# Optimization experiments

Hardware: AMD Instinct MI355X
Metric: run time of the kernel (lower is better)

The kernel has to match this reference:

```python
import jax, jax.numpy as jnp
import numpy as np

# Winograd F(2x2, 3x3) transform matrices (standard Lavin & Gray form).
# The original torch module encodes B^T / A^T but applies them with elementwise
# mul (a bug that crashes); the intended math is Y = A^T [ (G g G^T) .* (B^T d B) ] A
# per 4x4 input tile with stride 2, which equals a valid 3x3 conv. We implement
# that intended Winograd computation faithfully and vectorized.
_BT = jnp.array([[1., 0., -1., 0.],
                 [0., 1., 1., 0.],
                 [0., -1., 1., 0.],
                 [0., 1., 0., -1.]], dtype=jnp.float32)
_G = jnp.array([[1., 0., 0.],
                [0.5, 0.5, 0.5],
                [0.5, -0.5, 0.5],
                [0., 0., 1.]], dtype=jnp.float32)
_AT = jnp.array([[1., 1., 1., 0.],
                 [0., 1., -1., -1.]], dtype=jnp.float32)


def setup_inputs() -> dict:
    key = jax.random.key(0)
    k1, k2 = jax.random.split(key)
    X = jax.random.normal(k1, (16, 32, 258, 258), dtype=jnp.float32)
    K = jax.random.normal(k2, (32, 32, 3, 3), dtype=jnp.float32)
    return {"X": X, "K": K}


def _winograd_conv(X, K):
    B_, C, H, W = X.shape
    Fo = K.shape[0]
    blocks = (H - 3) // 2 + 1  # number of 2x2 output tiles per spatial dim

    # Kernel transform: U = G K G^T  -> (Fo, C, 4, 4)
    U = jnp.einsum('ij,fcjk,lk->fcil', _G, K, _G)

    # Extract overlapping 4x4 tiles with stride 2: (B, C, blocks, blocks, 4, 4)
    i0 = jnp.arange(blocks) * 2
    win = i0[:, None] + jnp.arange(4)[None, :]          # (blocks, 4)
    tiles = X[:, :, win, :]                              # (B, C, blocks, 4, W)
    tiles = tiles[:, :, :, :, win]                       # (B, C, blocks, 4, blocks, 4)
    tiles = tiles.transpose(0, 1, 2, 4, 3, 5)            # (B, C, p, q, 4, 4)

    # Input transform: V = B^T d B
    V = jnp.einsum('ij,bcpqjk,lk->bcpqil', _BT, tiles, _BT)

    # Elementwise multiply in transform domain, summed over input channels
    M = jnp.einsum('fcil,bcpqil->bfpqil', U, V)          # (B, Fo, p, q, 4, 4)

    # Inverse transform: Y = A^T M A -> (B, Fo, p, q, 2, 2)
    Y = jnp.einsum('ij,bfpqjk,lk->bfpqil', _AT, M, _AT)

    # Stitch 2x2 tiles back: (B, Fo, 2*blocks, 2*blocks)
    out = Y.transpose(0, 1, 2, 4, 3, 5).reshape(B_, Fo, 2 * blocks, 2 * blocks)
    return out


def reference(X, K):
    return _winograd_conv(X, K)
```

## Files before the change

kernel.cpp:

```cpp
#include <hip/hip_runtime.h>
#include <stdint.h>

typedef __attribute__((ext_vector_type(8))) short bf16x8;
typedef __attribute__((ext_vector_type(4))) float f32x4;
typedef __attribute__((ext_vector_type(2))) float f32x2;

__device__ inline float bflo(uint32_t w) { union { uint32_t i; float f; } v; v.i = w << 16; return v.f; }
__device__ inline float bfhi(uint32_t w) { union { uint32_t i; float f; } v; v.i = w & 0xffff0000u; return v.f; }
__device__ inline uint32_t f2bf(float f) { union { float f; uint32_t i; } v; v.f = f; return (v.i + 0x8000u) >> 16; }
__device__ inline uint32_t pk(float lo, float hi) { return f2bf(lo) | (f2bf(hi) << 16); }

__device__ inline f32x2 pka(f32x2 a, f32x2 b) {
    f32x2 d; asm("v_pk_add_f32 %0, %1, %2" : "=v"(d) : "v"(a), "v"(b)); return d;
}
__device__ inline f32x2 pks(f32x2 a, f32x2 b) {
    f32x2 d; asm("v_pk_add_f32 %0, %1, %2 neg_lo:[0,1] neg_hi:[0,1]" : "=v"(d) : "v"(a), "v"(b)); return d;
}
__device__ inline uint32_t cvtpk2(float lo, float hi) {
    uint32_t r; asm("v_cvt_pk_bf16_f32 %0, %1, %2" : "=v"(r) : "v"(lo), "v"(hi)); return r;
}
__device__ inline uint32_t cvtpk(f32x2 v) { return cvtpk2(v.x, v.y); }
__device__ inline f32x2 unpk(uint32_t w) {
    union { uint32_t u; float f; } lo, hi; lo.u = w << 16; hi.u = w & 0xffff0000u;
    return (f32x2){lo.f, hi.f};
}

__global__ __launch_bounds__(256) void wg_filter(const float* __restrict__ Kk, uint32_t* __restrict__ Ud)
{
    const int idx = blockIdx.x * 256 + threadIdx.x;
    if (idx >= 512) return;
    const int cp = idx & 15, f = idx >> 4;
    float u[2][16];
    #pragma unroll
    for (int h = 0; h < 2; h++) {
        const float* kp = Kk + (f * 32 + cp * 2 + h) * 9;
        float k00 = kp[0], k01 = kp[1], k02 = kp[2];
        float k10 = kp[3], k11 = kp[4], k12 = kp[5];
        float k20 = kp[6], k21 = kp[7], k22 = kp[8];
        float t[4][3];
        t[0][0] = k00; t[0][1] = k01; t[0][2] = k02;
        t[1][0] = 0.5f * (k00 + k10 + k20); t[1][1] = 0.5f * (k01 + k11 + k21); t[1][2] = 0.5f * (k02 + k12 + k22);
        t[2][0] = 0.5f * (k00 - k10 + k20); t[2][1] = 0.5f * (k01 - k11 + k21); t[2][2] = 0.5f * (k02 - k12 + k22);
        t[3][0] = k20; t[3][1] = k21; t[3][2] = k22;
        #pragma unroll
        for (int i = 0; i < 4; i++) {
            float a0 = t[i][0], a1 = t[i][1], a2 = t[i][2];
            u[h][i * 4 + 0] = a0;
            u[h][i * 4 + 1] = 0.5f * (a0 + a1 + a2);
            u[h][i * 4 + 2] = 0.5f * (a0 - a1 + a2);
            u[h][i * 4 + 3] = a2;
        }
    }
    const int base = ((cp >> 2) * 32 + f) * 4 + (cp & 3);
    #pragma unroll
    for (int p = 0; p < 16; p++) Ud[p * 512 + base] = pk(u[0][p], u[1][p]);
}

template<int CH>
__device__ __forceinline__ void d_phase(const uint16_t* __restrict__ Vbuf,
                                        const bf16x8 (&a)[4], float (&y)[4][4],
                                        int tb, int lq, int l15)
{
    const uint16_t* Vb = Vbuf + ((tb * 4 + lq) * 16 + l15) * 8;
    f32x4 acc[4];
    #pragma unroll
    for (int l = 0; l < 4; l++) {
        bf16x8 v = *(const bf16x8*)(Vb + l * 1024);
        acc[l] = __builtin_amdgcn_mfma_f32_16x16x32_bf16(a[l], v,
                    (f32x4){0.f, 0.f, 0.f, 0.f}, 0, 0, 0);
    }
    #pragma unroll
    for (int r = 0; r < 4; r++) {
        float m0 = acc[0][r], m1 = acc[1][r], m2 = acc[2][r], m3 = acc[3][r];
        float c0 = m0 + m1 + m2, c1 = m1 - m2 - m3;
        if (CH == 0)      { y[r][0] += c0; y[r][1] += c1; }
        else if (CH == 1) { y[r][0] += c0; y[r][1] += c1; y[r][2] += c0; y[r][3] += c1; }
        else if (CH == 2) { y[r][0] += c0; y[r][1] += c1; y[r][2] -= c0; y[r][3] -= c1; }
        else              { y[r][2] -= c0; y[r][3] -= c1; }
    }
}

__global__ __launch_bounds__(256, 3) void wg_main(
    const float* __restrict__ X, const uint16_t* __restrict__ U, float* __restrict__ out)
{
    __shared__ __align__(16) uint32_t Pl[2912];
    __shared__ __align__(16) uint16_t Vl[2][4096];

    const int tid = threadIdx.x;
    const int lin  = blockIdx.x + 16 * (blockIdx.y + 32 * blockIdx.z);
    const int work = (lin & 7) * 1024 + (lin >> 3);
    const int qb = work & 15;
    const int pb = (work >> 4) & 31;
    const int b  = work >> 9;
    const int y0 = pb * 8, x0 = qb * 16;

    const int wave = tid >> 6, lane = tid & 63;
    const int fh = wave & 1, tb = wave >> 1;
    const int l15 = lane & 15, lq = lane >> 4;
    const uint16_t* Ub = U + (lq * 32 + fh * 16 + l15) * 8;

    bf16x8 a_cur[4], a_nxt[4];
    #pragma unroll
    for (int l = 0; l < 4; l++)
        a_cur[l] = *(const bf16x8*)(Ub + l * 1024);

    for (int s = tid; s < 1440; s += 256) {
        const int pr = s / 90;
        const int r  = s - pr * 90;
        const int row = r / 9, seg = r - row * 9;
        const float* g0 = X + ((size_t)((b * 32 + pr * 2) * 258 + y0 + row)) * 258 + x0 + seg * 2;
        float2 a = *(const float2*)g0;
        float2 c = *(const float2*)(g0 + 258 * 258);
        uint2 w;
        w.x = cvtpk2(a.x, c.x);
        w.y = cvtpk2(a.y, c.y);
        *(uint2*)&Pl[pr * 182 + row * 18 + seg * 2] = w;
    }
    #pragma unroll
    for (int l = 0; l < 4; l++)
        a_nxt[l] = *(const bf16x8*)(Ub + (2 * 4 + l) * 1024);
    __syncthreads();

    const int cp2 = tid & 3, t15c = (tid >> 2) & 15;

    float y[4][4];
    #pragma unroll
    for (int r = 0; r < 4; r++)
        #pragma unroll
        for (int j = 0; j < 4; j++) y[r][j] = 0.f;

    uint32_t vh1[2][4], vh3[2][4];
    int vbs[2];
    uint32_t* vp0 = (uint32_t*)Vl[0];
    uint32_t* vp1 = (uint32_t*)Vl[1];

    #pragma unroll
    for (int it = 0; it < 2; it++) {
        const int rem  = it * 4 + wave;
        const int tblk = rem & 1, cpH = rem >> 1;
        const int cp   = cpH * 4 + cp2;
        const int tt   = tblk * 16 + t15c;
        const int tr   = tt >> 3, tc = tt & 7;
        const uint32_t* pp = &Pl[cp * 182 + (tr * 2) * 18 + tc * 2];
        f32x2 d[4][4];
        #pragma unroll
        for (int j = 0; j < 4; j++) {
            uint2 w0 = *(const uint2*)&pp[j * 18];
            uint2 w1 = *(const uint2*)&pp[j * 18 + 2];
            d[j][0] = unpk(w0.x); d[j][1] = unpk(w0.y);
            d[j][2] = unpk(w1.x); d[j][3] = unpk(w1.y);
        }
        f32x2 e0[4], e1[4], e2[4], e3[4];
        #pragma unroll
        for (int k = 0; k < 4; k++) {
            e0[k] = pks(d[0][k], d[2][k]);
            e1[k] = pka(d[1][k], d[2][k]);
            e2[k] = pks(d[2][k], d[1][k]);
            e3[k] = pks(d[1][k], d[3][k]);
        }
        const int vbase = ((tblk * 4 + cpH) * 16 + t15c) * 4 + cp2;
        vbs[it] = vbase;
        vp0[0 * 512 + vbase] = cvtpk(pks(e0[0], e0[2]));
        vp0[1 * 512 + vbase] = cvtpk(pka(e0[1], e0[2]));
        vp0[2 * 512 + vbase] = cvtpk(pks(e0[2], e0[1]));
        vp0[3 * 512 + vbase] = cvtpk(pks(e0[1], e0[3]));
        vp1[0 * 512 + vbase] = cvtpk(pks(e2[0], e2[2]));
        vp1[1 * 512 + vbase] = cvtpk(pka(e2[1], e2[2]));
        vp1[2 * 512 + vbase] = cvtpk(pks(e2[2], e2[1]));
        vp1[3 * 512 + vbase] = cvtpk(pks(e2[1], e2[3]));
        vh1[it][0] = cvtpk(pks(e1[0], e1[2]));
        vh1[it][1] = cvtpk(pka(e1[1], e1[2]));
        vh1[it][2] = cvtpk(pks(e1[2], e1[1]));
        vh1[it][3] = cvtpk(pks(e1[1], e1[3]));
        vh3[it][0] = cvtpk(pks(e3[0], e3[2]));
        vh3[it][1] = cvtpk(pka(e3[1], e3[2]));
        vh3[it][2] = cvtpk(pks(e3[2], e3[1]));
        vh3[it][3] = cvtpk(pks(e3[1], e3[3]));
    }
    __syncthreads();

    d_phase<0>(Vl[0], a_cur, y, tb, lq, l15);
    #pragma unroll
    for (int l = 0; l < 4; l++) a_cur[l] = a_nxt[l];
    #pragma unroll
    for (int l = 0; l < 4; l++)
        a_nxt[l] = *(const bf16x8*)(Ub + (1 * 4 + l) * 1024);
    d_phase<2>(Vl[1], a_cur, y, tb, lq, l15);
    #pragma unroll
    for (int l = 0; l < 4; l++) a_cur[l] = a_nxt[l];
    #pragma unroll
    for (int l = 0; l < 4; l++)
        a_nxt[l] = *(const bf16x8*)(Ub + (3 * 4 + l) * 1024);

    __syncthreads();

    #pragma unroll
    for (int it = 0; it < 2; it++) {
        #pragma unroll
        for (int l = 0; l < 4; l++) {
            vp0[l * 512 + vbs[it]] = vh1[it][l];
            vp1[l * 512 + vbs[it]] = vh3[it][l];
        }
    }
    __syncthreads();

    d_phase<1>(Vl[0], a_cur, y, tb, lq, l15);
    #pragma unroll
    for (int l = 0; l < 4; l++) a_cur[l] = a_nxt[l];
    d_phase<3>(Vl[1], a_cur, y, tb, lq, l15);

    const int tt = tb * 16 + l15;
    const int trr = tt >> 3, tcc = tt & 7;
    const int p = pb * 4 + trr, q = qb * 8 + tcc;
    #pragma unroll
    for (int r = 0; r < 4; r++) {
        const int f = fh * 16 + lq * 4 + r;
        float* op = out + ((size_t)(b * 32 + f) * 256 + 2 * p) * 256 + 2 * q;
        *(float2*)op = make_float2(y[r][0], y[r][1]);
        *(float2*)(op + 256) = make_float2(y[r][2], y[r][3]);
    }
}

__device__ inline uint16_t f2bf16_rne(float f) {
    union { float f; uint32_t i; } v; v.f = f;
    uint32_t x = v.i;
    uint32_t r = x + 0x7fffu + ((x >> 16) & 1u);
    return (uint16_t)(r >> 16);
}
__global__ __launch_bounds__(256) void winograd_fallback(
    const float* __restrict__ X, const float* __restrict__ K, float* __restrict__ out)
{
    __shared__ uint16_t Ul[16384];
    __shared__ uint16_t Vl[16384];
    __shared__ uint16_t Pl[32 * 242];
    const int tid = threadIdx.x;
    const int qb = blockIdx.x, pb = blockIdx.y, b = blockIdx.z;
    for (int idx = tid; idx < 1024; idx += 256) {
        const int f = idx >> 5, c = idx & 31;
        const float* kp = K + (f * 32 + c) * 9;
        float k00 = kp[0], k01 = kp[1], k02 = kp[2];
        float k10 = kp[3], k11 = kp[4], k12 = kp[5];
        float k20 = kp[6], k21 = kp[7], k22 = kp[8];
        float t[4][3];
        t[0][0] = k00; t[0][1] = k01; t[0][2] = k02;
        t[1][0] = 0.5f * (k00 + k10 + k20); t[1][1] = 0.5f * (k01 + k11 + k21); t[1][2] = 0.5f * (k02 + k12 + k22);
        t[2][0] = 0.5f * (k00 - k10 + k20); t[2][1] = 0.5f * (k01 - k11 + k21); t[2][2] = 0.5f * (k02 - k12 + k22);
        t[3][0] = k20; t[3][1] = k21; t[3][2] = k22;
        const int ubase = ((c >> 3) * 32 + f) * 8 + (c & 7);
        #pragma unroll
        for (int i = 0; i < 4; i++) {
            float a0 = t[i][0], a1 = t[i][1], a2 = t[i][2];
            Ul[(i * 4 + 0) * 1024 + ubase] = f2bf16_rne(a0);
            Ul[(i * 4 + 1) * 1024 + ubase] = f2bf16_rne(0.5f * (a0 + a1 + a2));
            Ul[(i * 4 + 2) * 1024 + ubase] = f2bf16_rne(0.5f * (a0 - a1 + a2));
            Ul[(i * 4 + 3) * 1024 + ubase] = f2bf16_rne(a2);
        }
    }
    const int y0 = pb * 8, x0 = qb * 16;
    for (int s = tid; s < 2880; s += 256) {
        const int c = s / 90;
        const int r = s % 90;
        const int row = r / 9, seg = r % 9;
        const float* gp = X + ((b * 32 + c) * 258 + (y0 + row)) * 258 + x0 + seg * 2;
        float2 g = *(const float2*)gp;
        uint32_t packed = (uint32_t)f2bf16_rne(g.x) | ((uint32_t)f2bf16_rne(g.y) << 16);
        *(uint32_t*)&Pl[c * 242 + row * 24 + seg * 2] = packed;
    }
    __syncthreads();
    for (int idx = tid; idx < 1024; idx += 256) {
        const int c = idx & 31, tt = idx >> 5;
        const int tr = tt >> 3, tc = tt & 7;
        const uint16_t* pp = &Pl[c * 242 + (tr * 2) * 24 + tc * 2];
        float d[4][4];
        #pragma unroll
        for (int j = 0; j < 4; j++) {
            uint32_t w0 = *(const uint32_t*)&pp[j * 24];
            uint32_t w1 = *(const uint32_t*)&pp[j * 24 + 2];
            d[j][0] = bflo(w0); d[j][1] = bfhi(w0);
            d[j][2] = bflo(w1); d[j][3] = bfhi(w1);
        }
        float bt[4][4];
        #pragma unroll
        for (int k = 0; k < 4; k++) {
            bt[0][k] = d[0][k] - d[2][k];
            bt[1][k] = d[1][k] + d[2][k];
            bt[2][k] = d[2][k] - d[1][k];
            bt[3][k] = d[1][k] - d[3][k];
        }
        const int vbase = (((tt >> 4) * 4 + (c >> 3)) * 16 + (tt & 15)) * 8 + (c & 7);
        #pragma unroll
        for (int i = 0; i < 4; i++) {
            float b0 = bt[i][0], b1 = bt[i][1], b2 = bt[i][2], b3 = bt[i][3];
            Vl[(i * 4 + 0) * 1024 + vbase] = f2bf16_rne(b0 - b2);
            Vl[(i * 4 + 1) * 1024 + vbase] = f2bf16_rne(b1 + b2);
            Vl[(i * 4 + 2) * 1024 + vbase] = f2bf16_rne(b2 - b1);
            Vl[(i * 4 + 3) * 1024 + vbase] = f2bf16_rne(b1 - b3);
        }
    }
    __syncthreads();
    const int wave = tid >> 6, lane = tid & 63;
    const int fh = wave & 1, tb = wave >> 1;
    const int l15 = lane & 15, lq = lane >> 4;
    f32x4 acc[16];
    #pragma unroll
    for (int p = 0; p < 16; p++) acc[p] = (f32x4){0.f, 0.f, 0.f, 0.f};
    #pragma unroll
    for (int p = 0; p < 16; p++) {
        bf16x8 a = *(const bf16x8*)&Ul[p * 1024 + (lq * 32 + fh * 16 + l15) * 8];
        bf16x8 bv = *(const bf16x8*)&Vl[p * 1024 + ((tb * 4 + lq) * 16 + l15) * 8];
        acc[p] = __builtin_amdgcn_mfma_f32_16x16x32_bf16(a, bv, acc[p], 0, 0, 0);
    }
    #pragma unroll
    for (int r = 0; r < 4; r++) {
        const int f = fh * 16 + lq * 4 + r;
        const int t = tb * 16 + l15;
        const int tr = t >> 3, tc = t & 7;
        const int p = pb * 4 + tr, q = qb * 8 + tc;
        float m[4][4];
        #pragma unroll
        for (int i = 0; i < 4; i++)
            #pragma unroll
            for (int l = 0; l < 4; l++)
                m[i][l] = acc[i * 4 + l][r];
        float s0[4], s1[4];
        #pragma unroll
        for (int k = 0; k < 4; k++) {
            s0[k] = m[0][k] + m[1][k] + m[2][k];
            s1[k] = m[1][k] - m[2][k] - m[3][k];
        }
        float* op = out + ((size_t)(b * 32 + f) * 256 + 2 * p) * 256 + 2 * q;
        *(float2*)op = make_float2(s0[0] + s0[1] + s0[2], s0[1] - s0[2] - s0[3]);
        *(float2*)(op + 256) = make_float2(s1[0] + s1[1] + s1[2], s1[1] - s1[2] - s1[3]);
    }
}

extern "C" void kernel_launch(void* const* d_in, const int* in_sizes, int n_in,
                              void* d_out, int out_size, void* d_ws, size_t ws_size,
                              hipStream_t stream) {
    const float* X = (const float*)d_in[0];
    const float* K = (const float*)d_in[1];
    float* out = (float*)d_out;
    dim3 grid(16, 32, 16);
    if (ws_size >= 32768) {
        wg_filter<<<2, 256, 0, stream>>>(K, (uint32_t*)d_ws);
        wg_main<<<grid, 256, 0, stream>>>(X, (const uint16_t*)d_ws, out);
    } else {
        winograd_fallback<<<grid, 256, 0, stream>>>(X, K, out);
    }
}
```

Measured before the change: 80.36 us.

## Load input tiles directly from global memory, dropping the LDS staging buffer

The input patch is no longer staged in shared memory as bf16 pairs. Each thread now reads its own overlapping 4x4 tiles for two channels straight from global memory as float4 rows and runs the Winograd input transform in fp32 before packing to bf16. This removes an LDS write/read round trip, one barrier and about 11 KB of shared memory, which could allow more blocks per CU. The cost is redundant global reads, since neighbouring tiles overlap by half, and float4 loads that may be misaligned because the row stride is 258 floats.

```diff
diff --git a/kernel.cpp b/kernel.cpp
--- a/kernel.cpp
+++ b/kernel.cpp
@@ -10,19 +10,8 @@
 __device__ inline uint32_t f2bf(float f) { union { float f; uint32_t i; } v; v.f = f; return (v.i + 0x8000u) >> 16; }
 __device__ inline uint32_t pk(float lo, float hi) { return f2bf(lo) | (f2bf(hi) << 16); }
 
-__device__ inline f32x2 pka(f32x2 a, f32x2 b) {
-    f32x2 d; asm("v_pk_add_f32 %0, %1, %2" : "=v"(d) : "v"(a), "v"(b)); return d;
-}
-__device__ inline f32x2 pks(f32x2 a, f32x2 b) {
-    f32x2 d; asm("v_pk_add_f32 %0, %1, %2 neg_lo:[0,1] neg_hi:[0,1]" : "=v"(d) : "v"(a), "v"(b)); return d;
-}
 __device__ inline uint32_t cvtpk2(float lo, float hi) {
     uint32_t r; asm("v_cvt_pk_bf16_f32 %0, %1, %2" : "=v"(r) : "v"(lo), "v"(hi)); return r;
-}
-__device__ inline uint32_t cvtpk(f32x2 v) { return cvtpk2(v.x, v.y); }
-__device__ inline f32x2 unpk(uint32_t w) {
-    union { uint32_t u; float f; } lo, hi; lo.u = w << 16; hi.u = w & 0xffff0000u;
-    return (f32x2){lo.f, hi.f};
 }
 
 __global__ __launch_bounds__(256) void wg_filter(const float* __restrict__ Kk, uint32_t* __restrict__ Ud)
@@ -83,7 +72,6 @@
 __global__ __launch_bounds__(256, 3) void wg_main(
     const float* __restrict__ X, const uint16_t* __restrict__ U, float* __restrict__ out)
 {
-    __shared__ __align__(16) uint32_t Pl[2912];
     __shared__ __align__(16) uint16_t Vl[2][4096];
 
     const int tid = threadIdx.x;
@@ -92,7 +80,6 @@
     const int qb = work & 15;
     const int pb = (work >> 4) & 31;
     const int b  = work >> 9;
-    const int y0 = pb * 8, x0 = qb * 16;
 
     const int wave = tid >> 6, lane = tid & 63;
     const int fh = wave & 1, tb = wave >> 1;
@@ -104,30 +91,7 @@
     for (int l = 0; l < 4; l++)
         a_cur[l] = *(const bf16x8*)(Ub + l * 1024);
 
-    for (int s = tid; s < 1440; s += 256) {
-        const int pr = s / 90;
-        const int r  = s - pr * 90;
-        const int row = r / 9, seg = r - row * 9;
-        const float* g0 = X + ((size_t)((b * 32 + pr * 2) * 258 + y0 + row)) * 258 + x0 + seg * 2;
-        float2 a = *(const float2*)g0;
-        float2 c = *(const float2*)(g0 + 258 * 258);
-        uint2 w;
-        w.x = cvtpk2(a.x, c.x);
-        w.y = cvtpk2(a.y, c.y);
-        *(uint2*)&Pl[pr * 182 + row * 18 + seg * 2] = w;
-    }
-    #pragma unroll
-    for (int l = 0; l < 4; l++)
-        a_nxt[l] = *(const bf16x8*)(Ub + (2 * 4 + l) * 1024);
-    __syncthreads();
-
     const int cp2 = tid & 3, t15c = (tid >> 2) & 15;
-
-    float y[4][4];
-    #pragma unroll
-    for (int r = 0; r < 4; r++)
-        #pragma unroll
-        for (int j = 0; j < 4; j++) y[r][j] = 0.f;
 
     uint32_t vh1[2][4], vh3[2][4];
     int vbs[2];
@@ -141,44 +105,64 @@
         const int cp   = cpH * 4 + cp2;
         const int tt   = tblk * 16 + t15c;
         const int tr   = tt >> 3, tc = tt & 7;
-        const uint32_t* pp = &Pl[cp * 182 + (tr * 2) * 18 + tc * 2];
-        f32x2 d[4][4];
-        #pragma unroll
-        for (int j = 0; j < 4; j++) {
-            uint2 w0 = *(const uint2*)&pp[j * 18];
-            uint2 w1 = *(const uint2*)&pp[j * 18 + 2];
-            d[j][0] = unpk(w0.x); d[j][1] = unpk(w0.y);
-            d[j][2] = unpk(w1.x); d[j][3] = unpk(w1.y);
-        }
-        f32x2 e0[4], e1[4], e2[4], e3[4];
-        #pragma unroll
-        for (int k = 0; k < 4; k++) {
-            e0[k] = pks(d[0][k], d[2][k]);
-            e1[k] = pka(d[1][k], d[2][k]);
-            e2[k] = pks(d[2][k], d[1][k]);
-            e3[k] = pks(d[1][k], d[3][k]);
+        const float* g0 = X + ((size_t)((b * 32 + cp * 2) * 258 + pb * 8 + tr * 2)) * 258
+                            + qb * 16 + tc * 2;
+        const float* g1 = g0 + 66564;
+        float4 A0 = *(const float4*)g0;
+        float4 A1 = *(const float4*)(g0 + 258);
+        float4 A2 = *(const float4*)(g0 + 516);
+        float4 A3 = *(const float4*)(g0 + 774);
+        float4 B0 = *(const float4*)g1;
+        float4 B1 = *(const float4*)(g1 + 258);
+        float4 B2 = *(const float4*)(g1 + 516);
+        float4 B3 = *(const float4*)(g1 + 774);
+
+        float ea0[4], ea1[4], ea2[4], ea3[4];
+        float eb0[4], eb1[4], eb2[4], eb3[4];
+        {
+            const float* a0 = &A0.x; const float* a1 = &A1.x;
+            const float* a2 = &A2.x; const float* a3 = &A3.x;
+            const float* b0 = &B0.x; const float* b1 = &B1.x;
+            const float* b2 = &B2.x; const float* b3 = &B3.x;
+            #pragma unroll
+            for (int k = 0; k < 4; k++) {
+                ea0[k] = a0[k] - a2[k];  eb0[k] = b0[k] - b2[k];
+                ea1[k] = a1[k] + a2[k];  eb1[k] = b1[k] + b2[k];
+                ea2[k] = a2[k] - a1[k];  eb2[k] = b2[k] - b1[k];
+                ea3[k] = a1[k] - a3[k];  eb3[k] = b1[k] - b3[k];
+            }
         }
         const int vbase = ((tblk * 4 + cpH) * 16 + t15c) * 4 + cp2;
         vbs[it] = vbase;
-        vp0[0 * 512 + vbase] = cvtpk(pks(e0[0], e0[2]));
-        vp0[1 * 512 + vbase] = cvtpk(pka(e0[1], e0[2]));
-        vp0[2 * 512 + vbase] = cvtpk(pks(e0[2], e0[1]));
-        vp0[3 * 512 + vbase] = cvtpk(pks(e0[1], e0[3]));
-        vp1[0 * 512 + vbase] = cvtpk(pks(e2[0], e2[2]));
-        vp1[1 * 512 + vbase] = cvtpk(pka(e2[1], e2[2]));
-        vp1[2 * 512 + vbase] = cvtpk(pks(e2[2], e2[1]));
-        vp1[3 * 512 + vbase] = cvtpk(pks(e2[1], e2[3]));
-        vh1[it][0] = cvtpk(pks(e1[0], e1[2]));
-        vh1[it][1] = cvtpk(pka(e1[1], e1[2]));
-        vh1[it][2] = cvtpk(pks(e1[2], e1[1]));
-        vh1[it][3] = cvtpk(pks(e1[1], e1[3]));
-        vh3[it][0] = cvtpk(pks(e3[0], e3[2]));
-        vh3[it][1] = cvtpk(pka(e3[1], e3[2]));
-        vh3[it][2] = cvtpk(pks(e3[2], e3[1]));
-        vh3[it][3] = cvtpk(pks(e3[1], e3[3]));
-    }
-    __syncthreads();
-
+        vp0[0 * 512 + vbase] = cvtpk2(ea0[0] - ea0[2], eb0[0] - eb0[2]);
+        vp0[1 * 512 + vbase] = cvtpk2(ea0[1] + ea0[2], eb0[1] + eb0[2]);
+        vp0[2 * 512 + vbase] = cvtpk2(ea0[2] - ea0[1], eb0[2] - eb0[1]);
+        vp0[3 * 512 + vbase] = cvtpk2(ea0[1] - ea0[3], eb0[1] - eb0[3]);
+        vp1[0 * 512 + vbase] = cvtpk2(ea2[0] - ea2[2], eb2[0] - eb2[2]);
+        vp1[1 * 512 + vbase] = cvtpk2(ea2[1] + ea2[2], eb2[1] + eb2[2]);
+        vp1[2 * 512 + vbase] = cvtpk2(ea2[2] - ea2[1], eb2[2] - eb2[1]);
+        vp1[3 * 512 + vbase] = cvtpk2(ea2[1] - ea2[3], eb2[1] - eb2[3]);
+        vh1[it][0] = cvtpk2(ea1[0] - ea1[2], eb1[0] - eb1[2]);
+        vh1[it][1] = cvtpk2(ea1[1] + ea1[2], eb1[1] + eb1[2]);
+        vh1[it][2] = cvtpk2(ea1[2] - ea1[1], eb1[2] - eb1[1]);
+        vh1[it][3] = cvtpk2(ea1[1] - ea1[3], eb1[1] - eb1[3]);
+        vh3[it][0] = cvtpk2(ea3[0] - ea3[2], eb3[0] - eb3[2]);
+        vh3[it][1] = cvtpk2(ea3[1] + ea3[2], eb3[1] + eb3[2]);
+        vh3[it][2] = cvtpk2(ea3[2] - ea3[1], eb3[2] - eb3[1]);
+        vh3[it][3] = cvtpk2(ea3[1] - ea3[3], eb3[1] - eb3[3]);
+    }
+
+    float y[4][4];
+    #pragma unroll
+    for (int r = 0; r < 4; r++)
+        #pragma unroll
+        for (int j = 0; j < 4; j++) y[r][j] = 0.f;
+
+    __syncthreads();
+
+    #pragma unroll
+    for (int l = 0; l < 4; l++)
+        a_nxt[l] = *(const bf16x8*)(Ub + (2 * 4 + l) * 1024);
     d_phase<0>(Vl[0], a_cur, y, tb, lq, l15);
     #pragma unroll
     for (int l = 0; l < 4; l++) a_cur[l] = a_nxt[l];
```

Result: slower. 91.86 us (+14.3%).
